# Performance work log

Measured on AMD Instinct MI355X. Metric: run time of the kernel, lower is better.

## Reference

```python
import jax, jax.numpy as jnp
import numpy as np

DIM = 2048
N_HEADS = 32
N_KV_HEADS = 8
HEAD_DIM = 64
REPEATS = N_HEADS // N_KV_HEADS
SLIDING_WINDOW = 1024
EPS = 1e-6
B, T = 2, 2048


def _alibi_slopes(n):
    # n_heads=32 is a power of 2
    r = 2.0 ** (-8.0 / n)
    return jnp.asarray([r ** i for i in range(n)], dtype=jnp.float32)


def _rms_norm(x, w, eps):
    # RMSNorm over the last (flattened heads*head_dim) axis
    var = jnp.mean(x * x, axis=-1, keepdims=True)
    return x * jax.lax.rsqrt(var + eps) * w


def setup_inputs() -> dict:
    key = jax.random.key(0)
    ks = jax.random.split(key, 6)
    s = 0.02
    return {
        "x": jax.random.normal(ks[0], (B, T, DIM), jnp.float32),
        "wq": jax.random.normal(ks[1], (N_HEADS * HEAD_DIM, DIM), jnp.float32) * s,
        "wk": jax.random.normal(ks[2], (N_KV_HEADS * HEAD_DIM, DIM), jnp.float32) * s,
        "wv": jax.random.normal(ks[3], (N_KV_HEADS * HEAD_DIM, DIM), jnp.float32) * s,
        "wo": jax.random.normal(ks[4], (DIM, N_HEADS * HEAD_DIM), jnp.float32) * s,
        "q_norm_w": jnp.ones((N_HEADS * HEAD_DIM,), jnp.float32),
        "k_norm_w": jnp.ones((N_KV_HEADS * HEAD_DIM,), jnp.float32),
    }


def reference(x, wq, wk, wv, wo, q_norm_w, k_norm_w):
    bsz, seqlen, _ = x.shape
    xq = _rms_norm(x @ wq.T, q_norm_w, EPS)
    xk = _rms_norm(x @ wk.T, k_norm_w, EPS)
    xv = x @ wv.T
    xq = xq.reshape(bsz, seqlen, N_HEADS, HEAD_DIM).transpose(0, 2, 1, 3)  # b h t d
    xk = xk.reshape(bsz, seqlen, N_KV_HEADS, HEAD_DIM).transpose(0, 2, 1, 3)
    xv = xv.reshape(bsz, seqlen, N_KV_HEADS, HEAD_DIM).transpose(0, 2, 1, 3)
    # GQA: repeat_interleave kv heads
    xk = jnp.repeat(xk, REPEATS, axis=1)
    xv = jnp.repeat(xv, REPEATS, axis=1)

    pos = jnp.arange(seqlen)
    dist = pos[None, :] - pos[:, None]                     # [t,s] = s - t (<=0 on causal side)
    slopes = _alibi_slopes(N_HEADS)
    alibi = slopes[:, None, None] * dist.astype(jnp.float32)  # [h,t,s]
    allowed = (dist <= 0) & (dist >= -SLIDING_WINDOW)      # causal + sliding window
    bias = jnp.where(allowed[None], alibi, -jnp.inf)       # [h,t,s]

    scale = 1.0 / jnp.sqrt(jnp.asarray(HEAD_DIM, jnp.float32))
    scores = jnp.einsum("bhtd,bhsd->bhts", xq, xk) * scale + bias[None]
    attn = jax.nn.softmax(scores, axis=-1)
    out = jnp.einsum("bhts,bhsd->bhtd", attn, xv)          # [b,h,t,d]
    out = out.transpose(0, 2, 1, 3).reshape(bsz, seqlen, N_HEADS * HEAD_DIM)
    return out @ wo.T
```

## Files before the change

kernel.cpp:

```cpp
#include <hip/hip_runtime.h>


typedef _Float16 f16;
typedef __attribute__((ext_vector_type(8))) _Float16 f16x8;
typedef __attribute__((ext_vector_type(4))) _Float16 f16x4;
typedef __attribute__((ext_vector_type(2))) _Float16 f16x2;
typedef __attribute__((ext_vector_type(4))) float f32x4;

#define T_ 2048
#define NH 32
#define NKV 8
#define HD 64
#define WINDOW 1024
#define EPS_ 1e-6f
#define LOG2E 1.44269504088896340736f
#define LDQKV 3072

__device__ inline void async16(void* lds, const void* g) {
  __builtin_amdgcn_global_load_lds(
      (const __attribute__((address_space(1))) unsigned int*)g,
      (__attribute__((address_space(3))) unsigned int*)lds, 16, 0, 0);
}

struct CvtArgs {
  const float* src[5];
  f16* dst[5];
  int n4[5];
};
__global__ __launch_bounds__(256) void cvt_multi(CvtArgs a) {
  const int seg = blockIdx.y;
  const float* in = a.src[seg];
  f16* out = a.dst[seg];
  const int n4 = a.n4[seg];
  for (int i = blockIdx.x * blockDim.x + threadIdx.x; i < n4;
       i += gridDim.x * blockDim.x) {
    float4 v = ((const float4*)in)[i];
    f16x4 o;
    o[0] = (f16)v.x; o[1] = (f16)v.y; o[2] = (f16)v.z; o[3] = (f16)v.w;
    ((f16x4*)out)[i] = o;
  }
}

#define DSRD(p, off) (*(const f16x8*)((p) + (off)))

__global__ __launch_bounds__(512, 1) void gemm_nt192(const f16* __restrict__ A,
                                                     const f16* __restrict__ B,
                                                     f16* __restrict__ C) {
  constexpr int K = 2048, ldc = 3072;
  extern __shared__ char smem[];
  f16* sA = (f16*)smem;
  f16* sB = (f16*)(smem + 65536);

  const int gx = gridDim.x;
  const int nwg = gx * gridDim.y;
  int bid = blockIdx.y * gx + blockIdx.x;
  bid = (bid & 7) * (nwg >> 3) + (bid >> 3);
  const int m0 = (bid / gx) * 256;
  const int n0 = (bid % gx) * 192;

  const int tid = threadIdx.x;
  const int lane = tid & 63;
  const int wave = tid >> 6;
  const int quad = lane >> 4, l16 = lane & 15;
  const int wm = wave >> 2, wn = wave & 3;

  const int srow = tid >> 3;
  const int sgr = (((tid & 7) ^ (srow & 7))) * 8;
  const f16* gA = A + (size_t)(m0 + srow) * K + sgr;
  const f16* gB = B + (size_t)(n0 + srow) * K + sgr;
  const size_t r64 = (size_t)64 * K;

  const char* cA = (const char*)sA;
  const char* cB = (const char*)sB;
  const int xm = (l16 & 7) << 4;
  const int xk0 = (quad * 16) ^ xm;
  const int xk1 = (64 + quad * 16) ^ xm;
  const int abase = (wm * 128 + l16) * 128;
  const int bbase = (wn * 48 + l16) * 128;

  f32x4 acc[8][3] = {};
  const int nt = K >> 6;

#pragma unroll
  for (int a = 0; a < 4; ++a)
    async16(sA + a * 4096 + tid * 8, gA + (size_t)a * r64);
#pragma unroll
  for (int rb = 0; rb < 3; ++rb)
    async16(sB + rb * 4096 + tid * 8, gB + (size_t)rb * r64);
  asm volatile("s_waitcnt vmcnt(0)" ::: "memory");
  __builtin_amdgcn_s_barrier();

  for (int t = 0; t < nt; ++t) {
    const int bufoA = (t & 1) << 15;
    const int bufoB = (t & 1) * 24576;
    const bool st = (t + 1 < nt);

    if (st) {
      f16* sAn = sA + (((t & 1) ^ 1) << 14);
      f16* sBn = sB + ((t & 1) ^ 1) * 12288;
      const size_t gk = (size_t)(t + 1) * 64;
#pragma unroll
      for (int a = 0; a < 4; ++a)
        async16(sAn + a * 4096 + tid * 8, gA + a * r64 + gk);
#pragma unroll
      for (int rb = 0; rb < 3; ++rb)
        async16(sBn + rb * 4096 + tid * 8, gB + rb * r64 + gk);
    }

    f16x8 bf[3][2];
#pragma unroll
    for (int j = 0; j < 3; ++j) {
      bf[j][0] = DSRD(cB, bufoB + bbase + j * 2048 + xk0);
      bf[j][1] = DSRD(cB, bufoB + bbase + j * 2048 + xk1);
    }
#pragma unroll
    for (int mh = 0; mh < 2; ++mh) {
      f16x8 a0[4], a1[4];
#pragma unroll
      for (int i = 0; i < 4; ++i) {
        a0[i] = DSRD(cA, bufoA + abase + mh * 8192 + i * 2048 + xk0);
        a1[i] = DSRD(cA, bufoA + abase + mh * 8192 + i * 2048 + xk1);
      }
#pragma unroll
      for (int i = 0; i < 4; ++i)
#pragma unroll
        for (int j = 0; j < 3; ++j) {
          acc[mh * 4 + i][j] = __builtin_amdgcn_mfma_f32_16x16x32_f16(
              a0[i], bf[j][0], acc[mh * 4 + i][j], 0, 0, 0);
          acc[mh * 4 + i][j] = __builtin_amdgcn_mfma_f32_16x16x32_f16(
              a1[i], bf[j][1], acc[mh * 4 + i][j], 0, 0, 0);
        }
    }

    if (st) {
      asm volatile("s_waitcnt vmcnt(0)" ::: "memory");
      __builtin_amdgcn_s_barrier();
    }
  }

#pragma unroll
  for (int im = 0; im < 8; ++im) {
    const int row0 = m0 + wm * 128 + im * 16 + quad * 4;
#pragma unroll
    for (int j = 0; j < 3; ++j) {
      const int col = n0 + wn * 48 + j * 16 + l16;
#pragma unroll
      for (int r = 0; r < 4; ++r)
        C[(size_t)(row0 + r) * ldc + col] = (f16)acc[im][j][r];
    }
  }
}

template <int BN>
__global__ __launch_bounds__(512, 2) void gemm_nt8(const f16* __restrict__ A,
                                                   const f16* __restrict__ B,
                                                   void* __restrict__ C,
                                                   int M, int N, int K, int ldc,
                                                   int out_f32) {
  constexpr int WN = BN / 4;
  constexpr int JN = WN / 32;
  constexpr int RB = BN / 64;
  constexpr int BUFB = BN * 128;
  extern __shared__ char smem[];
  f16* sA = (f16*)smem;
  f16* sB = (f16*)(smem + 65536);

  const int gx = gridDim.x;
  const int nwg = gx * gridDim.y;
  int bid = blockIdx.y * gx + blockIdx.x;
  if (!(nwg & 7)) bid = (bid & 7) * (nwg >> 3) + (bid >> 3);
  const int m0 = (bid / gx) * 256;
  const int n0 = (bid % gx) * BN;

  const int tid = threadIdx.x;
  const int lane = tid & 63;
  const int wave = tid >> 6;
  const int quad = lane >> 4, l16 = lane & 15;
  const int wm = wave >> 2, wn = wave & 3;

  const int srow = tid >> 3;
  const int sgr = (((tid & 7) ^ (srow & 7))) * 8;
  const f16* gA = A + (size_t)(m0 + srow) * K + sgr;
  const f16* gB = B + (size_t)(n0 + srow) * K + sgr;
  const size_t r64 = (size_t)64 * K;

  const char* cA = (const char*)sA;
  const char* cB = (const char*)sB;
  const int xm = (l16 & 7) << 4;
  const int xk0 = (quad * 16) ^ xm;
  const int xk1 = (64 + quad * 16) ^ xm;
  const int abase = (wm * 128 + l16) * 128;
  const int bbase = (wn * WN + l16) * 128;

  f32x4 acc[8][2 * JN] = {};
  const int nt = K >> 6;

#pragma unroll
  for (int a = 0; a < 4; ++a)
    async16(sA + a * 4096 + tid * 8, gA + (size_t)a * r64);
#pragma unroll
  for (int rb = 0; rb < RB; ++rb)
    async16(sB + rb * 4096 + tid * 8, gB + (size_t)rb * r64);
  asm volatile("s_waitcnt vmcnt(0)" ::: "memory");
  __builtin_amdgcn_s_barrier();

  for (int t = 0; t < nt; ++t) {
    const int bufoA = (t & 1) << 15;
    const int bufoB = (t & 1) * BUFB;
    const bool st = (t + 1 < nt);

    if (st) {
      f16* sAn = sA + (((t & 1) ^ 1) << 14);
      f16* sBn = sB + ((t & 1) ^ 1) * (BUFB / 2);
      const size_t gk = (size_t)(t + 1) * 64;
#pragma unroll
      for (int a = 0; a < 4; ++a)
        async16(sAn + a * 4096 + tid * 8, gA + a * r64 + gk);
#pragma unroll
      for (int rb = 0; rb < RB; ++rb)
        async16(sBn + rb * 4096 + tid * 8, gB + rb * r64 + gk);
    }

    f16x8 bf[2 * JN][2];
#pragma unroll
    for (int nh = 0; nh < 2; ++nh)
#pragma unroll
      for (int j = 0; j < JN; ++j) {
        bf[nh * JN + j][0] =
            DSRD(cB, bufoB + bbase + nh * (WN / 2) * 128 + j * 2048 + xk0);
        bf[nh * JN + j][1] =
            DSRD(cB, bufoB + bbase + nh * (WN / 2) * 128 + j * 2048 + xk1);
      }
#pragma unroll
    for (int mh = 0; mh < 2; ++mh) {
      f16x8 a0[4], a1[4];
#pragma unroll
      for (int i = 0; i < 4; ++i) {
        a0[i] = DSRD(cA, bufoA + abase + mh * 8192 + i * 2048 + xk0);
        a1[i] = DSRD(cA, bufoA + abase + mh * 8192 + i * 2048 + xk1);
      }
#pragma unroll
      for (int i = 0; i < 4; ++i)
#pragma unroll
        for (int j = 0; j < 2 * JN; ++j) {
          acc[mh * 4 + i][j] = __builtin_amdgcn_mfma_f32_16x16x32_f16(
              a0[i], bf[j][0], acc[mh * 4 + i][j], 0, 0, 0);
          acc[mh * 4 + i][j] = __builtin_amdgcn_mfma_f32_16x16x32_f16(
              a1[i], bf[j][1], acc[mh * 4 + i][j], 0, 0, 0);
        }
    }

    if (st) {
      asm volatile("s_waitcnt vmcnt(0)" ::: "memory");
      __builtin_amdgcn_s_barrier();
    }
  }

#pragma unroll
  for (int im = 0; im < 8; ++im) {
    const int row0 = m0 + wm * 128 + im * 16 + quad * 4;
#pragma unroll
    for (int jn = 0; jn < 2 * JN; ++jn) {
      const int col = n0 + wn * WN + jn * 16 + l16;
#pragma unroll
      for (int r = 0; r < 4; ++r) {
        const float v = acc[im][jn][r];
        if (out_f32) ((float*)C)[(size_t)(row0 + r) * ldc + col] = v;
        else         ((f16*)C)[(size_t)(row0 + r) * ldc + col] = (f16)v;
      }
    }
  }
}

__global__ __launch_bounds__(256) void rmsnorm2(f16* __restrict__ xqkv,
                                                const float* __restrict__ qw,
                                                const float* __restrict__ kw) {
  __shared__ float red[4];
  const int which = blockIdx.y;
  const int tid = threadIdx.x;

  auto block_sum = [&](float ss) -> float {
#pragma unroll
    for (int off = 32; off > 0; off >>= 1) ss += __shfl_down(ss, off);
    if ((tid & 63) == 0) red[tid >> 6] = ss;
    __syncthreads();
    return red[0] + red[1] + red[2] + red[3];
  };

  if (which == 0) {
    f16* p = xqkv + (size_t)blockIdx.x * LDQKV;
    f16x8 v = ((const f16x8*)p)[tid];
    float f[8];
    float ss = 0.f;
#pragma unroll
    for (int j = 0; j < 8; ++j) { f[j] = (float)v[j]; ss += f[j] * f[j]; }
    const float scale = rsqrtf(block_sum(ss) / 2048.0f + EPS_);
    const float4 w0 = ((const float4*)qw)[tid * 2];
    const float4 w1 = ((const float4*)qw)[tid * 2 + 1];
    f16x8 o;
    o[0] = (f16)(f[0] * scale * w0.x); o[1] = (f16)(f[1] * scale * w0.y);
    o[2] = (f16)(f[2] * scale * w0.z); o[3] = (f16)(f[3] * scale * w0.w);
    o[4] = (f16)(f[4] * scale * w1.x); o[5] = (f16)(f[5] * scale * w1.y);
    o[6] = (f16)(f[6] * scale * w1.z); o[7] = (f16)(f[7] * scale * w1.w);
    ((f16x8*)p)[tid] = o;
  } else {
    f16* p = xqkv + (size_t)blockIdx.x * LDQKV + 2048;
    f16x2 v = ((const f16x2*)p)[tid];
    const float f0 = (float)v[0], f1 = (float)v[1];
    const float scale = rsqrtf(block_sum(f0 * f0 + f1 * f1) / 512.0f + EPS_);
    const float2 w = ((const float2*)kw)[tid];
    f16x2 o;
    o[0] = (f16)(f0 * scale * w.x);
    o[1] = (f16)(f1 * scale * w.y);
    ((f16x2*)p)[tid] = o;
  }
}

__global__ __launch_bounds__(256) void kvfrag(const f16* __restrict__ xqkv,
                                              f16* __restrict__ Kf,
                                              f16* __restrict__ Vf) {
  __shared__ f16 Lk[64][72];
  __shared__ f16 Lv[64][72];
  const int kt = blockIdx.x;
  const int b = blockIdx.y >> 3, kh = blockIdx.y & 7;
  const int t0 = kt * 64;
  const int tid = threadIdx.x;
  const int r = tid >> 3, c = (tid & 7) * 8;
#pragma unroll
  for (int rp = 0; rp < 2; ++rp) {
    const int rr = r + rp * 32;
    const f16* src = xqkv + (size_t)(b * T_ + t0 + rr) * LDQKV + kh * 64 + c;
    *(f16x8*)(&Lk[rr][c]) = *(const f16x8*)(src + 2048);
    *(f16x8*)(&Lv[rr][c]) = *(const f16x8*)(src + 2560);
  }
  __syncthreads();
  const size_t obase = ((size_t)(b * 8 + kh) * 32 + kt) * 4096;
#pragma unroll
  for (int cc0 = 0; cc0 < 2; ++cc0) {
    const int cc = tid + cc0 * 256;
    const int nb = cc >> 7, kc = (cc >> 6) & 1, ln = cc & 63;
    const int qd = ln >> 4, s16 = ln & 15;
    *(f16x8*)(Kf + obase + cc * 8) = *(const f16x8*)(&Lk[nb * 16 + s16][kc * 32 + qd * 8]);
    f16x8 o;
#pragma unroll
    for (int j = 0; j < 8; ++j) o[j] = Lv[kc * 32 + qd * 8 + j][nb * 16 + s16];
    *(f16x8*)(Vf + obase + cc * 8) = o;
  }
}

__global__ __launch_bounds__(256, 4) void attn(const f16* __restrict__ Q,
                                               const f16* __restrict__ Kf,
                                               const f16* __restrict__ Vf,
                                               f16* __restrict__ O) {
  constexpr int LDW = 72;
  __shared__ f16 Qs[128 * LDW];
  __shared__ float Lx[4][2][16];

  const int qt2 = 15 - blockIdx.x;
  const int h = blockIdx.y, b = blockIdx.z;
  const int kh = h >> 2;
  const int q0 = qt2 * 128;
  const int tid = threadIdx.x;
  const int lane = tid & 63, wave = tid >> 6;
  const int quad = lane >> 4, l16 = lane & 15;
  const float scale2 = 0.125f * LOG2E;
  const float slope2 = exp2f(-0.25f * (float)h) * LOG2E;
  const float M2 = 10.0f;

  const int sr = tid >> 3, sc = (tid & 7) * 8;

#pragma unroll
  for (int rp = 0; rp < 4; ++rp) {
    const int rr = sr + rp * 32;
    *(f16x8*)(Qs + rr * LDW + sc) =
        *(const f16x8*)(Q + (size_t)(b * T_ + q0 + rr) * LDQKV + h * HD + sc);
  }
  __syncthreads();
  f16x8 qa[2], qb[2];
#pragma unroll
  for (int kc = 0; kc < 2; ++kc) {
    qa[kc] = *(const f16x8*)(Qs + (wave * 32 + l16) * LDW + kc * 32 + quad * 8);
    qb[kc] = *(const f16x8*)(Qs + (wave * 32 + 16 + l16) * LDW + kc * 32 + quad * 8);
  }
  f16* PsA = Qs + (wave * 32) * LDW;
  f16* PsB = Qs + (wave * 32 + 16) * LDW;

  f32x4 o0[4] = {}, o1[4] = {};
  float lsA = 0.f, lsB = 0.f;

  const int kt_lo = (q0 >= WINDOW) ? ((q0 - WINDOW) >> 6) : 0;
  const int kt_hi = (q0 + 127) >> 6;
  const int gA0 = q0 + wave * 32;
  const int gB0 = gA0 + 16;
  const int qA = gA0 + l16;
  const int qB = qA + 16;
  const f16* kfb = Kf + (size_t)(b * 8 + kh) * 131072 + lane * 8;
  const f16* vfb = Vf + (size_t)(b * 8 + kh) * 131072 + lane * 8;

  float sr4[4];
#pragma unroll
  for (int r = 0; r < 4; ++r) sr4[r] = slope2 * (float)r;
  float baseA = slope2 * (float)(kt_lo * 64 + quad * 4 - qA) - M2;
  float baseB = slope2 * (float)(kt_lo * 64 + quad * 4 - qB) - M2;
  const float bstep = slope2 * 64.0f;
  const float b16 = slope2 * 16.0f;

  for (int kt = kt_lo; kt <= kt_hi; ++kt) {
    const int k0 = kt * 64;
    const f16* kp = kfb + kt * 4096;
    const f16* vp = vfb + kt * 4096;
    const bool maskA = (k0 + 63 > gA0) || (k0 + WINDOW < gA0 + 15);
    const bool maskB = (k0 + 63 > gB0) || (k0 + WINDOW < gB0 + 15);

    float bnbA = baseA, bnbB = baseB;
#pragma unroll
    for (int nb = 0; nb < 4; ++nb) {
      const f16x8 k0f = *(const f16x8*)(kp + (nb * 2) * 512);
      const f16x8 k1f = *(const f16x8*)(kp + (nb * 2 + 1) * 512);
      f32x4 a = {0.f, 0.f, 0.f, 0.f};
      a = __builtin_amdgcn_mfma_f32_16x16x32_f16(k0f, qa[0], a, 0, 0, 0);
      a = __builtin_amdgcn_mfma_f32_16x16x32_f16(k1f, qa[1], a, 0, 0, 0);
      f32x4 c = {0.f, 0.f, 0.f, 0.f};
      c = __builtin_amdgcn_mfma_f32_16x16x32_f16(k0f, qb[0], c, 0, 0, 0);
      c = __builtin_amdgcn_mfma_f32_16x16x32_f16(k1f, qb[1], c, 0, 0, 0);

      f16x4 pkA, pkB;
#pragma unroll
      for (int r = 0; r < 4; ++r) {
        const int key = k0 + nb * 16 + quad * 4 + r;
        float vA = fmaf(a[r], scale2, bnbA + sr4[r]);
        if (maskA) {
          const int dist = key - qA;
          if (dist > 0 || dist < -WINDOW) vA = -1e30f;
        }
        const float pA = __builtin_amdgcn_exp2f(vA);
        lsA += pA;
        pkA[r] = (f16)pA;
        float vB = fmaf(c[r], scale2, bnbB + sr4[r]);
        if (maskB) {
          const int dist = key - qB;
          if (dist > 0 || dist < -WINDOW) vB = -1e30f;
        }
        const float pB = __builtin_amdgcn_exp2f(vB);
        lsB += pB;
        pkB[r] = (f16)pB;
      }
      *(f16x4*)(PsA + l16 * LDW + nb * 16 + quad * 4) = pkA;
      *(f16x4*)(PsB + l16 * LDW + nb * 16 + quad * 4) = pkB;
      bnbA += b16; bnbB += b16;
    }
    baseA += bstep; baseB += bstep;

    const f16x8 paA0 = *(const f16x8*)(PsA + l16 * LDW + quad * 8);
    const f16x8 paA1 = *(const f16x8*)(PsA + l16 * LDW + 32 + quad * 8);
    const f16x8 paB0 = *(const f16x8*)(PsB + l16 * LDW + quad * 8);
    const f16x8 paB1 = *(const f16x8*)(PsB + l16 * LDW + 32 + quad * 8);
#pragma unroll
    for (int nb = 0; nb < 4; ++nb) {
      const f16x8 v0 = *(const f16x8*)(vp + (nb * 2) * 512);
      const f16x8 v1 = *(const f16x8*)(vp + (nb * 2 + 1) * 512);
      o0[nb] = __builtin_amdgcn_mfma_f32_16x16x32_f16(paA0, v0, o0[nb], 0, 0, 0);
      o0[nb] = __builtin_amdgcn_mfma_f32_16x16x32_f16(paA1, v1, o0[nb], 0, 0, 0);
      o1[nb] = __builtin_amdgcn_mfma_f32_16x16x32_f16(paB0, v0, o1[nb], 0, 0, 0);
      o1[nb] = __builtin_amdgcn_mfma_f32_16x16x32_f16(paB1, v1, o1[nb], 0, 0, 0);
    }
  }

  lsA += __shfl_xor(lsA, 16);
  lsA += __shfl_xor(lsA, 32);
  lsB += __shfl_xor(lsB, 16);
  lsB += __shfl_xor(lsB, 32);
  if (quad == 0) { Lx[wave][0][l16] = lsA; Lx[wave][1][l16] = lsB; }
  float rlA[4], rlB[4];
#pragma unroll
  for (int r = 0; r < 4; ++r) {
    rlA[r] = 1.0f / Lx[wave][0][quad * 4 + r];
    rlB[r] = 1.0f / Lx[wave][1][quad * 4 + r];
  }

#pragma unroll
  for (int r = 0; r < 4; ++r) {
    const int qrA = q0 + wave * 32 + quad * 4 + r;
#pragma unroll
    for (int nb = 0; nb < 4; ++nb) {
      O[(size_t)(b * T_ + qrA) * (NH * HD) + h * HD + nb * 16 + l16] =
          (f16)(o0[nb][r] * rlA[r]);
      O[(size_t)(b * T_ + qrA + 16) * (NH * HD) + h * HD + nb * 16 + l16] =
          (f16)(o1[nb][r] * rlB[r]);
    }
  }
}

extern "C" void kernel_launch(void* const* d_in, const int* in_sizes, int n_in,
                              void* d_out, int out_size, void* d_ws, size_t ws_size,
                              hipStream_t stream) {
  const float* x  = (const float*)d_in[0];
  const float* wq = (const float*)d_in[1];
  const float* wk = (const float*)d_in[2];
  const float* wv = (const float*)d_in[3];
  const float* wo = (const float*)d_in[4];
  const float* qw = (const float*)d_in[5];
  const float* kw = (const float*)d_in[6];
  float* out = (float*)d_out;

  char* ws = (char*)d_ws;
  size_t off = 0;
  auto carve = [&](size_t bytes) -> char* {
    char* p = ws + off;
    off += (bytes + 255) & ~(size_t)255;
    return p;
  };
  f16* xh    = (f16*)carve((size_t)4096 * 2048 * 2);
  f16* wqkvh = (f16*)carve((size_t)3072 * 2048 * 2);
  f16* woh   = (f16*)carve((size_t)2048 * 2048 * 2);
  f16* xqkv  = (f16*)carve((size_t)4096 * 3072 * 2);
  f16* Kf = wqkvh;
  f16* Vf = wqkvh + (size_t)16 * 131072;
  f16* ao = xh;

  static bool attr_done = false;
  if (!attr_done) {
    (void)hipFuncSetAttribute((const void*)gemm_nt192,
                              hipFuncAttributeMaxDynamicSharedMemorySize,
                              114688);
    (void)hipFuncSetAttribute((const void*)gemm_nt8<128>,
                              hipFuncAttributeMaxDynamicSharedMemorySize,
                              98304);
    attr_done = true;
  }

  CvtArgs ca;
  ca.src[0] = x;  ca.dst[0] = xh;                            ca.n4[0] = (4096 * 2048) / 4;
  ca.src[1] = wq; ca.dst[1] = wqkvh;                         ca.n4[1] = (2048 * 2048) / 4;
  ca.src[2] = wk; ca.dst[2] = wqkvh + (size_t)2048 * 2048;   ca.n4[2] = (512 * 2048) / 4;
  ca.src[3] = wv; ca.dst[3] = wqkvh + (size_t)2560 * 2048;   ca.n4[3] = (512 * 2048) / 4;
  ca.src[4] = wo; ca.dst[4] = woh;                           ca.n4[4] = (2048 * 2048) / 4;
  cvt_multi<<<dim3(1024, 5), 256, 0, stream>>>(ca);

  gemm_nt192<<<dim3(16, 16), 512, 114688, stream>>>(xh, wqkvh, xqkv);
  rmsnorm2<<<dim3(4096, 2), 256, 0, stream>>>(xqkv, qw, kw);
  kvfrag<<<dim3(32, 16), 256, 0, stream>>>(xqkv, Kf, Vf);
  attn<<<dim3(16, 32, 2), 256, 0, stream>>>(xqkv, Kf, Vf, ao);
  gemm_nt8<128><<<dim3(16, 16), 512, 98304, stream>>>(ao, woh, out, 4096, 2048, 2048, 2048, 1);
}
```

Baseline: 281.7 us.

## Pre-swizzle QKV weights into MFMA fragment layout and load B directly from global

The fp32-to-fp16 conversion kernel now writes the Wq/Wk/Wv weights in a fragment-ordered layout that matches the MFMA B-operand register layout. The QKV GEMM then reads its B fragments straight from global memory into registers, with no LDS staging. This halves the GEMM's LDS footprint to 64KB and raises launch bounds to allow two workgroups per CU, removing B-tile LDS traffic. The trade-off is that B loads are now synchronous global loads inside the main loop with no prefetch, which may expose latency.

```diff
diff --git a/kernel.cpp b/kernel.cpp
--- a/kernel.cpp
+++ b/kernel.cpp
@@ -25,31 +25,52 @@
 struct CvtArgs {
   const float* src[5];
   f16* dst[5];
-  int n4[5];
+  int cnt[5];
+  int nofs[5];
+  int frag[5];
 };
 __global__ __launch_bounds__(256) void cvt_multi(CvtArgs a) {
   const int seg = blockIdx.y;
   const float* in = a.src[seg];
   f16* out = a.dst[seg];
-  const int n4 = a.n4[seg];
-  for (int i = blockIdx.x * blockDim.x + threadIdx.x; i < n4;
-       i += gridDim.x * blockDim.x) {
-    float4 v = ((const float4*)in)[i];
-    f16x4 o;
-    o[0] = (f16)v.x; o[1] = (f16)v.y; o[2] = (f16)v.z; o[3] = (f16)v.w;
-    ((f16x4*)out)[i] = o;
+  const int cnt = a.cnt[seg];
+  if (!a.frag[seg]) {
+    for (int i = blockIdx.x * blockDim.x + threadIdx.x; i < cnt;
+         i += gridDim.x * blockDim.x) {
+      float4 v = ((const float4*)in)[i];
+      f16x4 o;
+      o[0] = (f16)v.x; o[1] = (f16)v.y; o[2] = (f16)v.z; o[3] = (f16)v.w;
+      ((f16x4*)out)[i] = o;
+    }
+  } else {
+    const int nofs = a.nofs[seg];
+    for (int i = blockIdx.x * blockDim.x + threadIdx.x; i < cnt;
+         i += gridDim.x * blockDim.x) {
+      const float4 v0 = ((const float4*)in)[i * 2];
+      const float4 v1 = ((const float4*)in)[i * 2 + 1];
+      const int e = i * 8;
+      const int n = nofs + (e >> 11);
+      const int k = e & 2047;
+      const int n16 = n >> 4, l = n & 15;
+      const int kt = k >> 6, kc = (k >> 5) & 1, q = (k >> 3) & 3;
+      const size_t base =
+          ((((size_t)n16 * 32 + kt) * 2 + kc) * 512) + (size_t)(q * 16 + l) * 8;
+      f16x8 o;
+      o[0] = (f16)v0.x; o[1] = (f16)v0.y; o[2] = (f16)v0.z; o[3] = (f16)v0.w;
+      o[4] = (f16)v1.x; o[5] = (f16)v1.y; o[6] = (f16)v1.z; o[7] = (f16)v1.w;
+      *(f16x8*)(out + base) = o;
+    }
   }
 }
 
 #define DSRD(p, off) (*(const f16x8*)((p) + (off)))
 
-__global__ __launch_bounds__(512, 1) void gemm_nt192(const f16* __restrict__ A,
-                                                     const f16* __restrict__ B,
+__global__ __launch_bounds__(512, 2) void gemm_nt192(const f16* __restrict__ A,
+                                                     const f16* __restrict__ Bf,
                                                      f16* __restrict__ C) {
   constexpr int K = 2048, ldc = 3072;
   extern __shared__ char smem[];
   f16* sA = (f16*)smem;
-  f16* sB = (f16*)(smem + 65536);
 
   const int gx = gridDim.x;
   const int nwg = gx * gridDim.y;
@@ -67,16 +88,16 @@
   const int srow = tid >> 3;
   const int sgr = (((tid & 7) ^ (srow & 7))) * 8;
   const f16* gA = A + (size_t)(m0 + srow) * K + sgr;
-  const f16* gB = B + (size_t)(n0 + srow) * K + sgr;
   const size_t r64 = (size_t)64 * K;
 
   const char* cA = (const char*)sA;
-  const char* cB = (const char*)sB;
   const int xm = (l16 & 7) << 4;
   const int xk0 = (quad * 16) ^ xm;
   const int xk1 = (64 + quad * 16) ^ xm;
   const int abase = (wm * 128 + l16) * 128;
-  const int bbase = (wn * 48 + l16) * 128;
+
+  const int nb16 = (n0 >> 4) + wn * 3;
+  const f16* gBf = Bf + (size_t)lane * 8;
 
   f32x4 acc[8][3] = {};
   const int nt = K >> 6;
@@ -84,35 +105,29 @@
 #pragma unroll
   for (int a = 0; a < 4; ++a)
     async16(sA + a * 4096 + tid * 8, gA + (size_t)a * r64);
-#pragma unroll
-  for (int rb = 0; rb < 3; ++rb)
-    async16(sB + rb * 4096 + tid * 8, gB + (size_t)rb * r64);
   asm volatile("s_waitcnt vmcnt(0)" ::: "memory");
   __builtin_amdgcn_s_barrier();
 
   for (int t = 0; t < nt; ++t) {
     const int bufoA = (t & 1) << 15;
-    const int bufoB = (t & 1) * 24576;
     const bool st = (t + 1 < nt);
 
     if (st) {
       f16* sAn = sA + (((t & 1) ^ 1) << 14);
-      f16* sBn = sB + ((t & 1) ^ 1) * 12288;
       const size_t gk = (size_t)(t + 1) * 64;
 #pragma unroll
       for (int a = 0; a < 4; ++a)
         async16(sAn + a * 4096 + tid * 8, gA + a * r64 + gk);
-#pragma unroll
-      for (int rb = 0; rb < 3; ++rb)
-        async16(sBn + rb * 4096 + tid * 8, gB + rb * r64 + gk);
     }
 
     f16x8 bf[3][2];
 #pragma unroll
-    for (int j = 0; j < 3; ++j) {
-      bf[j][0] = DSRD(cB, bufoB + bbase + j * 2048 + xk0);
-      bf[j][1] = DSRD(cB, bufoB + bbase + j * 2048 + xk1);
-    }
+    for (int j = 0; j < 3; ++j)
+#pragma unroll
+      for (int kc = 0; kc < 2; ++kc)
+        bf[j][kc] = *(const f16x8*)(
+            gBf + ((((size_t)(nb16 + j) * 32 + t) * 2 + kc) * 512));
+
 #pragma unroll
     for (int mh = 0; mh < 2; ++mh) {
       f16x8 a0[4], a1[4];
@@ -522,7 +537,7 @@
   if (!attr_done) {
     (void)hipFuncSetAttribute((const void*)gemm_nt192,
                               hipFuncAttributeMaxDynamicSharedMemorySize,
-                              114688);
+                              65536);
     (void)hipFuncSetAttribute((const void*)gemm_nt8<128>,
                               hipFuncAttributeMaxDynamicSharedMemorySize,
                               98304);
@@ -530,14 +545,14 @@
   }
 
   CvtArgs ca;
-  ca.src[0] = x;  ca.dst[0] = xh;                            ca.n4[0] = (4096 * 2048) / 4;
-  ca.src[1] = wq; ca.dst[1] = wqkvh;                         ca.n4[1] = (2048 * 2048) / 4;
-  ca.src[2] = wk; ca.dst[2] = wqkvh + (size_t)2048 * 2048;   ca.n4[2] = (512 * 2048) / 4;
-  ca.src[3] = wv; ca.dst[3] = wqkvh + (size_t)2560 * 2048;   ca.n4[3] = (512 * 2048) / 4;
-  ca.src[4] = wo; ca.dst[4] = woh;                           ca.n4[4] = (2048 * 2048) / 4;
+  ca.src[0] = x;  ca.dst[0] = xh;    ca.cnt[0] = (4096 * 2048) / 4; ca.nofs[0] = 0;    ca.frag[0] = 0;
+  ca.src[1] = wq; ca.dst[1] = wqkvh; ca.cnt[1] = (2048 * 2048) / 8; ca.nofs[1] = 0;    ca.frag[1] = 1;
+  ca.src[2] = wk; ca.dst[2] = wqkvh; ca.cnt[2] = (512 * 2048) / 8;  ca.nofs[2] = 2048; ca.frag[2] = 1;
+  ca.src[3] = wv; ca.dst[3] = wqkvh; ca.cnt[3] = (512 * 2048) / 8;  ca.nofs[3] = 2560; ca.frag[3] = 1;
+  ca.src[4] = wo; ca.dst[4] = woh;   ca.cnt[4] = (2048 * 2048) / 4; ca.nofs[4] = 0;    ca.frag[4] = 0;
   cvt_multi<<<dim3(1024, 5), 256, 0, stream>>>(ca);
 
-  gemm_nt192<<<dim3(16, 16), 512, 114688, stream>>>(xh, wqkvh, xqkv);
+  gemm_nt192<<<dim3(16, 16), 512, 65536, stream>>>(xh, wqkvh, xqkv);
   rmsnorm2<<<dim3(4096, 2), 256, 0, stream>>>(xqkv, qw, kw);
   kvfrag<<<dim3(32, 16), 256, 0, stream>>>(xqkv, Kf, Vf);
   attn<<<dim3(16, 32, 2), 256, 0, stream>>>(xqkv, Kf, Vf, ao);
```

New measurement: 299.2 us. +6.2%, slower.
